# Kernel optimization log

Measured on AMD Instinct MI355X. Metric: run time of the kernel, lower is better.

## Reference

```python
import jax, jax.numpy as jnp
import numpy as np

N = 50000          # num nodes
DEG = 16           # fixed degree (uniform CSR)
E = N * DEG        # num edges
R = 8              # num relations
IN = 128
HID = 128
OUT = 40
BN_EPS = 1e-5


def setup_inputs() -> dict:
    key = jax.random.key(0)
    k = jax.random.split(key, 5)
    x = jax.random.normal(k[0], (N, IN), jnp.float32)
    # glorot-ish init for per-relation weights
    W1 = jax.random.normal(k[1], (R, IN, HID), jnp.float32) * (2.0 / (IN + HID)) ** 0.5
    W2 = jax.random.normal(k[2], (R, HID, OUT), jnp.float32) * (2.0 / (HID + OUT)) ** 0.5
    ptr = jnp.arange(N + 1, dtype=jnp.int32) * DEG            # CSR row offsets
    idx = jax.random.randint(k[3], (E,), 0, N, jnp.int32)     # neighbor (src) ids
    edge_types = jax.random.randint(k[4], (E,), 0, R, jnp.int32)
    return {
        "x": x, "W1": W1, "W2": W2,
        "bn_gamma": jnp.ones((HID,), jnp.float32),
        "bn_beta": jnp.zeros((HID,), jnp.float32),
        "bn_mean": jnp.zeros((HID,), jnp.float32),
        "bn_var": jnp.ones((HID,), jnp.float32),
        "ptr": ptr, "idx": idx, "edge_types": edge_types,
    }


def _rgcn_layer(h, W, ptr, idx, edge_types):
    # RGCNOP: out[i] = sum_{e in [ptr[i],ptr[i+1])} x[idx[e]] @ W[etype[e]]
    # Efficient form: transform every node by every relation once, then gather
    # the (src, etype) pair per edge and scatter-add into destinations.
    xr = jnp.einsum('nd,rdh->nrh', h, W)             # [N, R, H]
    msgs = xr[idx, edge_types]                       # [E, H] irregular gather
    deg = ptr[1:] - ptr[:-1]                         # [N]
    dst = jnp.repeat(jnp.arange(ptr.shape[0] - 1, dtype=jnp.int32), deg,
                     total_repeat_length=idx.shape[0])
    agg = jax.ops.segment_sum(msgs, dst, num_segments=ptr.shape[0] - 1)
    return agg / deg[:, None].astype(agg.dtype)      # degree normalization


def reference(x, W1, W2, bn_gamma, bn_beta, bn_mean, bn_var, ptr, idx, edge_types):
    h = _rgcn_layer(x, W1, ptr, idx, edge_types)
    # BatchNorm1d in eval mode (history_size=0, dropout inactive)
    h = (h - bn_mean) * jax.lax.rsqrt(bn_var + BN_EPS) * bn_gamma + bn_beta
    h = jax.nn.relu(h)
    h = _rgcn_layer(h, W2, ptr, idx, edge_types)
    return jax.nn.log_softmax(h, axis=-1)
```

## Files before the change

### kernel.cpp

```cpp
#include <hip/hip_runtime.h>
#include <math.h>

typedef __attribute__((ext_vector_type(8))) short bf16x8;
typedef __attribute__((ext_vector_type(4))) float f32x4;

constexpr int kN   = 50000;
constexpr int kR   = 8;
constexpr int kIn  = 128;
constexpr int kHid = 128;
constexpr int kOut = 40;
constexpr int kNT  = 16;
constexpr int kLds = 1032;
constexpr float kBnEps = 1e-5f;

__device__ inline ushort f2bf(float x) {
    uint u = __float_as_uint(x);
    u += 0x7FFFu + ((u >> 16) & 1u);
    return (ushort)(u >> 16);
}
__device__ inline float bf2f(ushort s) { return __uint_as_float(((uint)s) << 16); }
__device__ inline ushort f2bf_c(float x) {
    return (ushort)((__float_as_uint(x) + 0x8000u) >> 16);
}


__global__ __launch_bounds__(256)
void prep_new(const float* __restrict__ x,  ushort* __restrict__ xb,
              const float* __restrict__ W1, ushort* __restrict__ W1p,
              const float* __restrict__ W2, ushort* __restrict__ W2p)
{
    const int b   = blockIdx.x;
    const int tid = threadIdx.x;
    if (b < 3125) {
        const size_t i = ((size_t)b * 256 + tid) * 8;
        const float4 v0 = *(const float4*)&x[i];
        const float4 v1 = *(const float4*)&x[i + 4];
        *(ushort4*)&xb[i]     = make_ushort4(f2bf(v0.x), f2bf(v0.y), f2bf(v0.z), f2bf(v0.w));
        *(ushort4*)&xb[i + 4] = make_ushort4(f2bf(v1.x), f2bf(v1.y), f2bf(v1.z), f2bf(v1.w));
        return;
    }
    const int lane = tid & 63;
    const int m = lane & 15, q = lane >> 4;
    ushort hv[8];
    if (b < 3125 + 64) {
        const int f  = (b - 3125) * 4 + (tid >> 6);
        const int nt = f >> 2, kt = f & 3;
        const int n  = nt * 16 + m;
        const int r  = n >> 7, h = n & 127;
        #pragma unroll
        for (int j = 0; j < 8; ++j) {
            const int k = kt * 32 + q * 8 + j;
            hv[j] = f2bf(W1[(size_t)r * 16384 + (size_t)k * 128 + h]);
        }
        const size_t o = ((size_t)f * 64 + lane) * 8;
        *(ushort4*)&W1p[o]     = make_ushort4(hv[0], hv[1], hv[2], hv[3]);
        *(ushort4*)&W1p[o + 4] = make_ushort4(hv[4], hv[5], hv[6], hv[7]);
    } else {
        const int f  = (b - 3189) * 4 + (tid >> 6);
        const int nt = f >> 2, kt = f & 3;
        const int n  = nt * 16 + m;
        const int r  = n >> 6, h = n & 63;
        #pragma unroll
        for (int j = 0; j < 8; ++j) {
            const int k = kt * 32 + q * 8 + j;
            hv[j] = (h < kOut) ? f2bf(W2[(size_t)r * 5120 + (size_t)k * 40 + h])
                               : (ushort)0;
        }
        const size_t o = ((size_t)f * 64 + lane) * 8;
        *(ushort4*)&W2p[o]     = make_ushort4(hv[0], hv[1], hv[2], hv[3]);
        *(ushort4*)&W2p[o + 4] = make_ushort4(hv[4], hv[5], hv[6], hv[7]);
    }
}

#define LOADA(MT,KT) const bf16x8 af##MT##KT = \
    *(const bf16x8*)&As[MT * 16 + m][KT * 32 + q * 8];

template<int NTW, int NCOLS>
__global__ __launch_bounds__(512, 4)
void xform(const ushort* __restrict__ in,
           const ushort* __restrict__ Bp,
           ushort* __restrict__ outp)
{
    __shared__ ushort As[64][136];
    const int tid  = threadIdx.x;
    const int base = blockIdx.x * 64;

    {
        const int row = tid >> 3, c = tid & 7;
        const int gr  = base + row;
        bf16x8 v0 = {0,0,0,0,0,0,0,0}, v1 = {0,0,0,0,0,0,0,0};
        if (gr < kN) {
            v0 = *(const bf16x8*)&in[(size_t)gr * 128 + c * 8];
            v1 = *(const bf16x8*)&in[(size_t)gr * 128 + c * 8 + 64];
        }
        *(bf16x8*)&As[row][c * 8]      = v0;
        *(bf16x8*)&As[row][c * 8 + 64] = v1;
    }
    __syncthreads();

    const int lane = tid & 63, wid = tid >> 6;
    const int m = lane & 15, q = lane >> 4;

    LOADA(0,0) LOADA(0,1) LOADA(0,2) LOADA(0,3)
    LOADA(1,0) LOADA(1,1) LOADA(1,2) LOADA(1,3)
    LOADA(2,0) LOADA(2,1) LOADA(2,2) LOADA(2,3)
    LOADA(3,0) LOADA(3,1) LOADA(3,2) LOADA(3,3)

    const bf16x8* B8 = (const bf16x8*)Bp;

    #pragma unroll
    for (int ii = 0; ii < NTW; ++ii) {
        const int nt = wid * NTW + ii;
        const bf16x8 b0 = B8[(size_t)(nt * 4 + 0) * 64 + lane];
        const bf16x8 b1 = B8[(size_t)(nt * 4 + 1) * 64 + lane];
        const bf16x8 b2 = B8[(size_t)(nt * 4 + 2) * 64 + lane];
        const bf16x8 b3 = B8[(size_t)(nt * 4 + 3) * 64 + lane];
        f32x4 c0 = {0.f,0.f,0.f,0.f}, c1 = {0.f,0.f,0.f,0.f};
        f32x4 c2 = {0.f,0.f,0.f,0.f}, c3 = {0.f,0.f,0.f,0.f};
        c0 = __builtin_amdgcn_mfma_f32_16x16x32_bf16(af00, b0, c0, 0, 0, 0);
        c1 = __builtin_amdgcn_mfma_f32_16x16x32_bf16(af10, b0, c1, 0, 0, 0);
        c2 = __builtin_amdgcn_mfma_f32_16x16x32_bf16(af20, b0, c2, 0, 0, 0);
        c3 = __builtin_amdgcn_mfma_f32_16x16x32_bf16(af30, b0, c3, 0, 0, 0);
        c0 = __builtin_amdgcn_mfma_f32_16x16x32_bf16(af01, b1, c0, 0, 0, 0);
        c1 = __builtin_amdgcn_mfma_f32_16x16x32_bf16(af11, b1, c1, 0, 0, 0);
        c2 = __builtin_amdgcn_mfma_f32_16x16x32_bf16(af21, b1, c2, 0, 0, 0);
        c3 = __builtin_amdgcn_mfma_f32_16x16x32_bf16(af31, b1, c3, 0, 0, 0);
        c0 = __builtin_amdgcn_mfma_f32_16x16x32_bf16(af02, b2, c0, 0, 0, 0);
        c1 = __builtin_amdgcn_mfma_f32_16x16x32_bf16(af12, b2, c1, 0, 0, 0);
        c2 = __builtin_amdgcn_mfma_f32_16x16x32_bf16(af22, b2, c2, 0, 0, 0);
        c3 = __builtin_amdgcn_mfma_f32_16x16x32_bf16(af32, b2, c3, 0, 0, 0);
        c0 = __builtin_amdgcn_mfma_f32_16x16x32_bf16(af03, b3, c0, 0, 0, 0);
        c1 = __builtin_amdgcn_mfma_f32_16x16x32_bf16(af13, b3, c1, 0, 0, 0);
        c2 = __builtin_amdgcn_mfma_f32_16x16x32_bf16(af23, b3, c2, 0, 0, 0);
        c3 = __builtin_amdgcn_mfma_f32_16x16x32_bf16(af33, b3, c3, 0, 0, 0);

        const int col = nt * 16 + m;
        #define STORE_MT(CC, MT) {                                          \
            const int r0 = base + MT * 16 + q * 4;                          \
            _Pragma("unroll")                                               \
            for (int i2 = 0; i2 < 4; ++i2) {                                \
                const int rr = r0 + i2;                                     \
                if (rr < kN)                                                \
                    outp[(size_t)rr * NCOLS + col] = f2bf_c(CC[i2]);        \
            } }
        STORE_MT(c0, 0) STORE_MT(c1, 1) STORE_MT(c2, 2) STORE_MT(c3, 3)
        #undef STORE_MT
    }
}

#define GADD(BV, GJ) \
    const uint BV = xrU[(size_t)(GJ) * 64 + lane]; \
    ax += __uint_as_float((BV) << 16); \
    ay += __uint_as_float((BV) & 0xffff0000u);

__global__ __launch_bounds__(512, 4)
void agg_bn(const ushort* __restrict__ xr1,
            const int* __restrict__ ptr, const int* __restrict__ idx,
            const int* __restrict__ etype,
            const float* __restrict__ gamma, const float* __restrict__ beta,
            const float* __restrict__ mean,  const float* __restrict__ var,
            ushort* __restrict__ h1b)
{
    const int lane = threadIdx.x & 63;
    const int wid  = threadIdx.x >> 6;
    const int node = blockIdx.x * 8 + wid;
    const int p0 = ptr[node], p1 = ptr[node + 1];
    const int deg = p1 - p0;
    const uint* xrU = (const uint*)xr1;

    float ax = 0.f, ay = 0.f;
    if (deg == 16) {
        const int gv = (idx[p0 + (lane & 15)] << 3) | etype[p0 + (lane & 15)];
        const int g0  = __builtin_amdgcn_readlane(gv, 0);
        const int g1  = __builtin_amdgcn_readlane(gv, 1);
        const int g2  = __builtin_amdgcn_readlane(gv, 2);
        const int g3  = __builtin_amdgcn_readlane(gv, 3);
        const int g4  = __builtin_amdgcn_readlane(gv, 4);
        const int g5  = __builtin_amdgcn_readlane(gv, 5);
        const int g6  = __builtin_amdgcn_readlane(gv, 6);
        const int g7  = __builtin_amdgcn_readlane(gv, 7);
        const int g8  = __builtin_amdgcn_readlane(gv, 8);
        const int g9  = __builtin_amdgcn_readlane(gv, 9);
        const int g10 = __builtin_amdgcn_readlane(gv, 10);
        const int g11 = __builtin_amdgcn_readlane(gv, 11);
        const int g12 = __builtin_amdgcn_readlane(gv, 12);
        const int g13 = __builtin_amdgcn_readlane(gv, 13);
        const int g14 = __builtin_amdgcn_readlane(gv, 14);
        const int g15 = __builtin_amdgcn_readlane(gv, 15);
        GADD(b0,  g0)  GADD(b1,  g1)  GADD(b2,  g2)  GADD(b3,  g3)
        GADD(b4,  g4)  GADD(b5,  g5)  GADD(b6,  g6)  GADD(b7,  g7)
        GADD(b8,  g8)  GADD(b9,  g9)  GADD(b10, g10) GADD(b11, g11)
        GADD(b12, g12) GADD(b13, g13) GADD(b14, g14) GADD(b15, g15)
    } else {
        for (int e = p0; e < p1; ++e) {
            const int src = __builtin_amdgcn_readfirstlane(idx[e]);
            const int et  = __builtin_amdgcn_readfirstlane(etype[e]);
            const uint b  = xrU[((size_t)src * 8 + et) * 64 + lane];
            ax += __uint_as_float(b << 16);
            ay += __uint_as_float(b & 0xffff0000u);
        }
    }

    const float invd = 1.0f / (float)deg;
    const int c0 = lane * 2;
    const float2 gm = *(const float2*)&gamma[c0];
    const float2 bt = *(const float2*)&beta[c0];
    const float2 mu = *(const float2*)&mean[c0];
    const float2 vr = *(const float2*)&var[c0];
    float v0 = (ax * invd - mu.x) * (gm.x * rsqrtf(vr.x + kBnEps)) + bt.x;
    float v1 = (ay * invd - mu.y) * (gm.y * rsqrtf(vr.y + kBnEps)) + bt.y;
    v0 = fmaxf(v0, 0.f);
    v1 = fmaxf(v1, 0.f);
    const uint px = (__float_as_uint(v0) + 0x8000u) >> 16;
    const uint py = (__float_as_uint(v1) + 0x8000u) & 0xffff0000u;
    ((uint*)h1b)[(size_t)node * 64 + lane] = px | py;
}

#define GADD2(BV, GJ) \
    const uint BV = xrU[(size_t)(GJ) * 32 + lane]; \
    ax += __uint_as_float((BV) << 16); \
    ay += __uint_as_float((BV) & 0xffff0000u);

__global__ __launch_bounds__(512, 4)
void agg_sm(const ushort* __restrict__ xr2,
            const int* __restrict__ ptr, const int* __restrict__ idx,
            const int* __restrict__ etype,
            float* __restrict__ out)
{
    const int lane = threadIdx.x & 63;
    const int wid  = threadIdx.x >> 6;
    const int node = blockIdx.x * 8 + wid;
    const int p0 = ptr[node], p1 = ptr[node + 1];
    const int deg = p1 - p0;
    const uint* xrU = (const uint*)xr2;

    float ax = 0.f, ay = 0.f;
    if (deg == 16) {
        const int gv = (idx[p0 + (lane & 15)] << 3) | etype[p0 + (lane & 15)];
        const int g0  = __builtin_amdgcn_readlane(gv, 0);
        const int g1  = __builtin_amdgcn_readlane(gv, 1);
        const int g2  = __builtin_amdgcn_readlane(gv, 2);
        const int g3  = __builtin_amdgcn_readlane(gv, 3);
        const int g4  = __builtin_amdgcn_readlane(gv, 4);
        const int g5  = __builtin_amdgcn_readlane(gv, 5);
        const int g6  = __builtin_amdgcn_readlane(gv, 6);
        const int g7  = __builtin_amdgcn_readlane(gv, 7);
        const int g8  = __builtin_amdgcn_readlane(gv, 8);
        const int g9  = __builtin_amdgcn_readlane(gv, 9);
        const int g10 = __builtin_amdgcn_readlane(gv, 10);
        const int g11 = __builtin_amdgcn_readlane(gv, 11);
        const int g12 = __builtin_amdgcn_readlane(gv, 12);
        const int g13 = __builtin_amdgcn_readlane(gv, 13);
        const int g14 = __builtin_amdgcn_readlane(gv, 14);
        const int g15 = __builtin_amdgcn_readlane(gv, 15);
        if (lane < 20) {
            GADD2(b0,  g0)  GADD2(b1,  g1)  GADD2(b2,  g2)  GADD2(b3,  g3)
            GADD2(b4,  g4)  GADD2(b5,  g5)  GADD2(b6,  g6)  GADD2(b7,  g7)
            GADD2(b8,  g8)  GADD2(b9,  g9)  GADD2(b10, g10) GADD2(b11, g11)
            GADD2(b12, g12) GADD2(b13, g13) GADD2(b14, g14) GADD2(b15, g15)
        }
    } else {
        for (int e = p0; e < p1; ++e) {
            const int src = __builtin_amdgcn_readfirstlane(idx[e]);
            const int et  = __builtin_amdgcn_readfirstlane(etype[e]);
            if (lane < 20) {
                const uint b = xrU[((size_t)src * 8 + et) * 32 + lane];
                ax += __uint_as_float(b << 16);
                ay += __uint_as_float(b & 0xffff0000u);
            }
        }
    }

    const float invd = 1.0f / (float)deg;
    ax *= invd; ay *= invd;

    float mx = (lane < 20) ? fmaxf(ax, ay) : -INFINITY;
    #pragma unroll
    for (int off = 32; off > 0; off >>= 1)
        mx = fmaxf(mx, __shfl_xor(mx, off, 64));
    float s = (lane < 20) ? (__expf(ax - mx) + __expf(ay - mx)) : 0.f;
    #pragma unroll
    for (int off = 32; off > 0; off >>= 1)
        s += __shfl_xor(s, off, 64);
    const float ls = __logf(s);
    if (lane < 20) {
        float2 o;
        o.x = ax - mx - ls;
        o.y = ay - mx - ls;
        *(float2*)&out[(size_t)node * kOut + lane * 2] = o;
    }
}


__device__ __forceinline__ void pack_unit(const float* __restrict__ W,
                                          ushort* __restrict__ dst,
                                          int N, int frag, int lane)
{
    const int kt = frag & 31;
    const int nt = frag >> 5;
    const int n  = nt * 16 + (lane & 15);
    const int q  = lane >> 4;
    ushort hv[8];
    #pragma unroll
    for (int j = 0; j < 8; ++j) {
        const int k = kt * 32 + q * 8 + j;
        hv[j] = f2bf((n < N) ? W[(size_t)k * N + n] : 0.f);
    }
    const size_t o = ((size_t)frag * 64 + lane) * 8;
    *(ushort4*)&dst[o]     = make_ushort4(hv[0], hv[1], hv[2], hv[3]);
    *(ushort4*)&dst[o + 4] = make_ushort4(hv[4], hv[5], hv[6], hv[7]);
}

__global__ __launch_bounds__(256)
void prep_old(const float* __restrict__ x,  ushort* __restrict__ xb,
              const float* __restrict__ W1, ushort* __restrict__ W1hi,
              const float* __restrict__ W2, ushort* __restrict__ W2hi)
{
    const int b   = blockIdx.x;
    const int tid = threadIdx.x;
    if (b < 3125) {
        const size_t i = ((size_t)b * 256 + tid) * 8;
        const float4 v0 = *(const float4*)&x[i];
        const float4 v1 = *(const float4*)&x[i + 4];
        *(ushort4*)&xb[i]     = make_ushort4(f2bf(v0.x), f2bf(v0.y), f2bf(v0.z), f2bf(v0.w));
        *(ushort4*)&xb[i + 4] = make_ushort4(f2bf(v1.x), f2bf(v1.y), f2bf(v1.z), f2bf(v1.w));
    } else if (b < 3125 + 64) {
        pack_unit(W1, W1hi, kHid, (b - 3125) * 4 + (tid >> 6), tid & 63);
    } else {
        const int frag = (b - 3189) * 4 + (tid >> 6);
        if (frag < 96) pack_unit(W2, W2hi, kOut, frag, tid & 63);
    }
}

#define ACCUM_ET(ET, VX, VY)                                   \
    if      ((ET) == 0) { a0.x += (VX); a0.y += (VY); }        \
    else if ((ET) == 1) { a1.x += (VX); a1.y += (VY); }        \
    else if ((ET) == 2) { a2.x += (VX); a2.y += (VY); }        \
    else if ((ET) == 3) { a3.x += (VX); a3.y += (VY); }        \
    else if ((ET) == 4) { a4.x += (VX); a4.y += (VY); }        \
    else if ((ET) == 5) { a5.x += (VX); a5.y += (VY); }        \
    else if ((ET) == 6) { a6.x += (VX); a6.y += (VY); }        \
    else                { a7.x += (VX); a7.y += (VY); }

#define GATHER(BV, SRC) \
    const ushort2 BV = *(const ushort2*)&feat[(size_t)(SRC) * 128 + d2];

#define ACCUM_EDGE(J, BV) \
    { const int et = __builtin_amdgcn_readlane(ve, J); ACCUM_ET(et, bf2f(BV.x), bf2f(BV.y)) }

#define STORE_AGG(RR, AV) \
    *(ushort2*)&aggHi[n][(RR) * 128 + d2] = make_ushort2(f2bf(AV.x), f2bf(AV.y));

__device__ __forceinline__ void phaseA_bf16(const ushort* __restrict__ feat,
                                            const int* __restrict__ ptr,
                                            const int* __restrict__ idx,
                                            const int* __restrict__ etype,
                                            int base, ushort (*aggHi)[kLds])
{
    const int lane = threadIdx.x & 63;
    const int wid  = threadIdx.x >> 6;
    const int d2   = lane * 2;

    #pragma unroll
    for (int t = 0; t < 2; ++t) {
        const int n    = wid * 2 + t;
        const int node = base + n;
        const int p0   = ptr[node];
        const int deg  = ptr[node + 1] - p0;

        float2 a0 = {0.f,0.f}, a1 = {0.f,0.f}, a2 = {0.f,0.f}, a3 = {0.f,0.f};
        float2 a4 = {0.f,0.f}, a5 = {0.f,0.f}, a6 = {0.f,0.f}, a7 = {0.f,0.f};

        if (deg == 16) {
            const int vi = idx[p0 + (lane & 15)];
            const int ve = etype[p0 + (lane & 15)];
            const int s0  = __builtin_amdgcn_readlane(vi, 0);
            const int s1  = __builtin_amdgcn_readlane(vi, 1);
            const int s2  = __builtin_amdgcn_readlane(vi, 2);
            const int s3  = __builtin_amdgcn_readlane(vi, 3);
            const int s4  = __builtin_amdgcn_readlane(vi, 4);
            const int s5  = __builtin_amdgcn_readlane(vi, 5);
            const int s6  = __builtin_amdgcn_readlane(vi, 6);
            const int s7  = __builtin_amdgcn_readlane(vi, 7);
            const int s8  = __builtin_amdgcn_readlane(vi, 8);
            const int s9  = __builtin_amdgcn_readlane(vi, 9);
            const int s10 = __builtin_amdgcn_readlane(vi, 10);
            const int s11 = __builtin_amdgcn_readlane(vi, 11);
            const int s12 = __builtin_amdgcn_readlane(vi, 12);
            const int s13 = __builtin_amdgcn_readlane(vi, 13);
            const int s14 = __builtin_amdgcn_readlane(vi, 14);
            const int s15 = __builtin_amdgcn_readlane(vi, 15);
            GATHER(b0,  s0)  GATHER(b1,  s1)  GATHER(b2,  s2)  GATHER(b3,  s3)
            GATHER(b4,  s4)  GATHER(b5,  s5)  GATHER(b6,  s6)  GATHER(b7,  s7)
            GATHER(b8,  s8)  GATHER(b9,  s9)  GATHER(b10, s10) GATHER(b11, s11)
            GATHER(b12, s12) GATHER(b13, s13) GATHER(b14, s14) GATHER(b15, s15)
            ACCUM_EDGE(0,  b0)  ACCUM_EDGE(1,  b1)  ACCUM_EDGE(2,  b2)  ACCUM_EDGE(3,  b3)
            ACCUM_EDGE(4,  b4)  ACCUM_EDGE(5,  b5)  ACCUM_EDGE(6,  b6)  ACCUM_EDGE(7,  b7)
            ACCUM_EDGE(8,  b8)  ACCUM_EDGE(9,  b9)  ACCUM_EDGE(10, b10) ACCUM_EDGE(11, b11)
            ACCUM_EDGE(12, b12) ACCUM_EDGE(13, b13) ACCUM_EDGE(14, b14) ACCUM_EDGE(15, b15)
        } else {
            for (int e = p0; e < p0 + deg; ++e) {
                const int src = __builtin_amdgcn_readfirstlane(idx[e]);
                const int et  = __builtin_amdgcn_readfirstlane(etype[e]);
                const ushort2 u = *(const ushort2*)&feat[(size_t)src * 128 + d2];
                ACCUM_ET(et, bf2f(u.x), bf2f(u.y))
            }
        }
        STORE_AGG(0, a0) STORE_AGG(1, a1) STORE_AGG(2, a2) STORE_AGG(3, a3)
        STORE_AGG(4, a4) STORE_AGG(5, a5) STORE_AGG(6, a6) STORE_AGG(7, a7)
    }
}

__global__ __launch_bounds__(512, 4)
void rgcn_layer1(const ushort* __restrict__ xb,
                 const ushort* __restrict__ W1hi,
                 const float* __restrict__ gamma, const float* __restrict__ beta,
                 const float* __restrict__ mean,  const float* __restrict__ var,
                 const int* __restrict__ ptr, const int* __restrict__ idx,
                 const int* __restrict__ etype,
                 ushort* __restrict__ h1b)
{
    __shared__ ushort aggHi[kNT][kLds];
    const int tid  = threadIdx.x;
    const int base = blockIdx.x * kNT;

    phaseA_bf16(xb, ptr, idx, etype, base, aggHi);
    __syncthreads();

    const int lane = tid & 63;
    const int wid  = tid >> 6;
    const int m    = lane & 15;
    const int q    = lane >> 4;

    const bf16x8* Bh = (const bf16x8*)W1hi + (size_t)wid * 32 * 64 + lane;
    f32x4 acc = {0.f, 0.f, 0.f, 0.f};

    #pragma unroll 4
    for (int kt = 0; kt < 32; ++kt) {
        const bf16x8 ah = *(const bf16x8*)&aggHi[m][kt * 32 + q * 8];
        const bf16x8 bh = Bh[(size_t)kt * 64];
        acc = __builtin_amdgcn_mfma_f32_16x16x32_bf16(ah, bh, acc, 0, 0, 0);
    }

    const int c = wid * 16 + m;
    const float g  = gamma[c] * rsqrtf(var[c] + kBnEps);
    const float mu = mean[c];
    const float bt = beta[c];
    #pragma unroll
    for (int i = 0; i < 4; ++i) {
        const int node = base + q * 4 + i;
        const float invdeg = 1.0f / (float)(ptr[node + 1] - ptr[node]);
        float v = (acc[i] * invdeg - mu) * g + bt;
        v = fmaxf(v, 0.f);
        h1b[(size_t)node * kHid + c] = f2bf(v);
    }
}

__global__ __launch_bounds__(512, 4)
void rgcn_layer2(const ushort* __restrict__ h1b,
                 const ushort* __restrict__ W2hi,
                 const int* __restrict__ ptr, const int* __restrict__ idx,
                 const int* __restrict__ etype,
                 float* __restrict__ out)
{
    __shared__ ushort aggHi[kNT][kLds];
    __shared__ float logits[kNT][48];
    const int tid  = threadIdx.x;
    const int base = blockIdx.x * kNT;

    phaseA_bf16(h1b, ptr, idx, etype, base, aggHi);
    __syncthreads();

    const int lane = tid & 63;
    const int wid  = tid >> 6;
    const int m    = lane & 15;
    const int q    = lane >> 4;

    if (wid < 3) {
        const bf16x8* Bh = (const bf16x8*)W2hi + (size_t)wid * 32 * 64 + lane;
        f32x4 acc = {0.f, 0.f, 0.f, 0.f};
        #pragma unroll 4
        for (int kt = 0; kt < 32; ++kt) {
            const bf16x8 ah = *(const bf16x8*)&aggHi[m][kt * 32 + q * 8];
            const bf16x8 bh = Bh[(size_t)kt * 64];
            acc = __builtin_amdgcn_mfma_f32_16x16x32_bf16(ah, bh, acc, 0, 0, 0);
        }
        const int n = wid * 16 + m;
        if (n < kOut) {
            #pragma unroll
            for (int i = 0; i < 4; ++i) {
                const int node = base + q * 4 + i;
                const float invdeg = 1.0f / (float)(ptr[node + 1] - ptr[node]);
                logits[q * 4 + i][n] = acc[i] * invdeg;
            }
        }
    }
    __syncthreads();

    #pragma unroll
    for (int i = 0; i < 2; ++i) {
        const int nrow = wid * 2 + i;
        const int node = base + nrow;
        const float v = (lane < kOut) ? logits[nrow][lane] : -INFINITY;
        float mx = v;
        #pragma unroll
        for (int off = 32; off > 0; off >>= 1)
            mx = fmaxf(mx, __shfl_xor(mx, off, 64));
        float s = (lane < kOut) ? __expf(v - mx) : 0.f;
        #pragma unroll
        for (int off = 32; off > 0; off >>= 1)
            s += __shfl_xor(s, off, 64);
        if (lane < kOut)
            out[(size_t)node * kOut + lane] = v - mx - __logf(s);
    }
}

extern "C" void kernel_launch(void* const* d_in, const int* in_sizes, int n_in,
                              void* d_out, int out_size, void* d_ws, size_t ws_size,
                              hipStream_t stream)
{
    const float* x     = (const float*)d_in[0];
    const float* W1    = (const float*)d_in[1];
    const float* W2    = (const float*)d_in[2];
    const float* gamma = (const float*)d_in[3];
    const float* beta  = (const float*)d_in[4];
    const float* mean  = (const float*)d_in[5];
    const float* var   = (const float*)d_in[6];
    const int*   ptr   = (const int*)d_in[7];
    const int*   idx   = (const int*)d_in[8];
    const int*   et    = (const int*)d_in[9];
    float*       out   = (float*)d_out;

    char* ws = (char*)d_ws;
    constexpr size_t kNeedNew = 128393216;

    if (ws_size >= kNeedNew) {
        ushort* xb  = (ushort*)ws;
        ushort* h1b = (ushort*)(ws + 12800000);
        ushort* W1p = (ushort*)(ws + 25600000);
        ushort* W2p = (ushort*)(ws + 25862144);
        ushort* xr  = (ushort*)(ws + 25993216);

        prep_new<<<dim3(3125 + 64 + 32), dim3(256), 0, stream>>>(x, xb, W1, W1p, W2, W2p);
        xform<8, 1024><<<dim3(782), dim3(512), 0, stream>>>(xb, W1p, xr);
        agg_bn<<<dim3(6250), dim3(512), 0, stream>>>(xr, ptr, idx, et,
                                                     gamma, beta, mean, var, h1b);
        xform<4, 512><<<dim3(782), dim3(512), 0, stream>>>(h1b, W2p, xr);
        agg_sm<<<dim3(6250), dim3(512), 0, stream>>>(xr, ptr, idx, et, out);
    } else {
        ushort* h1b  = (ushort*)ws;
        ushort* xb   = (ushort*)(ws + 12800000);
        ushort* W1hi = (ushort*)(ws + 25600000);
        ushort* W2hi = (ushort*)(ws + 25600000 + 262144);

        prep_old<<<dim3(3125 + 64 + 24), dim3(256), 0, stream>>>(x, xb, W1, W1hi, W2, W2hi);
        dim3 grid(kN / kNT), block(512);
        rgcn_layer1<<<grid, block, 0, stream>>>(xb, W1hi, gamma, beta, mean, var,
                                                ptr, idx, et, h1b);
        rgcn_layer2<<<grid, block, 0, stream>>>(h1b, W2hi, ptr, idx, et, out);
    }
}
```

Baseline: 212.9 us.

## Stage xform outputs through LDS for coalesced stores; two nodes per wave in agg_bn

The transform kernel now writes MFMA results into a padded LDS tile and then stores each 128-column slab to global memory as 16-byte vectors per thread, replacing scattered 2-byte stores. Its column-tile loop is reordered so all eight waves cover one contiguous 128-column slab per iteration. The first aggregation kernel handles two nodes per wave, issuing 32 independent gathers before accumulating, which raises memory-level parallelism and halves the grid. The cost is two block barriers per slab in xform, extra LDS, and higher register pressure in agg_bn.

```diff
diff --git a/kernel.cpp b/kernel.cpp
--- a/kernel.cpp
+++ b/kernel.cpp
@@ -3,6 +3,7 @@
 
 typedef __attribute__((ext_vector_type(8))) short bf16x8;
 typedef __attribute__((ext_vector_type(4))) float f32x4;
+typedef __attribute__((ext_vector_type(2))) unsigned long long u64x2;
 
 constexpr int kN   = 50000;
 constexpr int kR   = 8;
@@ -75,13 +76,16 @@
 #define LOADA(MT,KT) const bf16x8 af##MT##KT = \
     *(const bf16x8*)&As[MT * 16 + m][KT * 32 + q * 8];
 
-template<int NTW, int NCOLS>
-__global__ __launch_bounds__(512, 4)
-void xform(const ushort* __restrict__ in,
-           const ushort* __restrict__ Bp,
-           ushort* __restrict__ outp)
-{
+template<int NCOLS>
+__device__ __forceinline__ void xform_body(const ushort* __restrict__ in,
+                                           const ushort* __restrict__ Bp,
+                                           ushort* __restrict__ outp)
+{
+    constexpr int G = NCOLS / 128;
     __shared__ ushort As[64][136];
+    __shared__ unsigned long long Cs64[64 * 33];
+    ushort* Cs = (ushort*)Cs64;
+
     const int tid  = threadIdx.x;
     const int base = blockIdx.x * 64;
 
@@ -107,10 +111,12 @@
     LOADA(3,0) LOADA(3,1) LOADA(3,2) LOADA(3,3)
 
     const bf16x8* B8 = (const bf16x8*)Bp;
-
-    #pragma unroll
-    for (int ii = 0; ii < NTW; ++ii) {
-        const int nt = wid * NTW + ii;
+    const int srow = tid >> 3, scc = (tid & 7) * 16;
+    const int sgr  = base + srow;
+
+    #pragma unroll 1
+    for (int ii = 0; ii < G; ++ii) {
+        const int nt = ii * 8 + wid;
         const bf16x8 b0 = B8[(size_t)(nt * 4 + 0) * 64 + lane];
         const bf16x8 b1 = B8[(size_t)(nt * 4 + 1) * 64 + lane];
         const bf16x8 b2 = B8[(size_t)(nt * 4 + 2) * 64 + lane];
@@ -134,24 +140,43 @@
         c2 = __builtin_amdgcn_mfma_f32_16x16x32_bf16(af23, b3, c2, 0, 0, 0);
         c3 = __builtin_amdgcn_mfma_f32_16x16x32_bf16(af33, b3, c3, 0, 0, 0);
 
-        const int col = nt * 16 + m;
-        #define STORE_MT(CC, MT) {                                          \
-            const int r0 = base + MT * 16 + q * 4;                          \
-            _Pragma("unroll")                                               \
-            for (int i2 = 0; i2 < 4; ++i2) {                                \
-                const int rr = r0 + i2;                                     \
-                if (rr < kN)                                                \
-                    outp[(size_t)rr * NCOLS + col] = f2bf_c(CC[i2]);        \
-            } }
-        STORE_MT(c0, 0) STORE_MT(c1, 1) STORE_MT(c2, 2) STORE_MT(c3, 3)
-        #undef STORE_MT
-    }
-}
-
-#define GADD(BV, GJ) \
-    const uint BV = xrU[(size_t)(GJ) * 64 + lane]; \
-    ax += __uint_as_float((BV) << 16); \
-    ay += __uint_as_float((BV) & 0xffff0000u);
+        #pragma unroll
+        for (int i2 = 0; i2 < 4; ++i2) {
+            Cs[(0 * 16 + q * 4 + i2) * 132 + wid * 16 + m] = f2bf_c(c0[i2]);
+            Cs[(1 * 16 + q * 4 + i2) * 132 + wid * 16 + m] = f2bf_c(c1[i2]);
+            Cs[(2 * 16 + q * 4 + i2) * 132 + wid * 16 + m] = f2bf_c(c2[i2]);
+            Cs[(3 * 16 + q * 4 + i2) * 132 + wid * 16 + m] = f2bf_c(c3[i2]);
+        }
+        __syncthreads();
+        const unsigned long long* s =
+            (const unsigned long long*)&Cs[srow * 132 + scc];
+        const unsigned long long v0_ = s[0], v1_ = s[1], v2_ = s[2], v3_ = s[3];
+        __syncthreads();
+        if (sgr < kN) {
+            unsigned long long* d =
+                (unsigned long long*)&outp[(size_t)sgr * NCOLS + ii * 128 + scc];
+            u64x2 p0; p0.x = v0_; p0.y = v1_;
+            u64x2 p1; p1.x = v2_; p1.y = v3_;
+            *(u64x2*)d       = p0;
+            *(u64x2*)(d + 2) = p1;
+        }
+    }
+}
+
+__global__ __launch_bounds__(512, 4)
+void xform_l1(const ushort* __restrict__ in, const ushort* __restrict__ Bp,
+              ushort* __restrict__ outp)
+{ xform_body<1024>(in, Bp, outp); }
+
+__global__ __launch_bounds__(512, 4)
+void xform_l2(const ushort* __restrict__ in, const ushort* __restrict__ Bp,
+              ushort* __restrict__ outp)
+{ xform_body<512>(in, Bp, outp); }
+
+#define RLG(J)  const int g##J = __builtin_amdgcn_readlane(gv, J);
+#define LDU(B, J) const uint B = xrU[(size_t)g##J * 64 + lane];
+#define ACC2(AX, AY, B) { AX += __uint_as_float((B) << 16); \
+                          AY += __uint_as_float((B) & 0xffff0000u); }
 
 __global__ __launch_bounds__(512, 4)
 void agg_bn(const ushort* __restrict__ xr1,
@@ -163,57 +188,74 @@
 {
     const int lane = threadIdx.x & 63;
     const int wid  = threadIdx.x >> 6;
-    const int node = blockIdx.x * 8 + wid;
-    const int p0 = ptr[node], p1 = ptr[node + 1];
-    const int deg = p1 - p0;
+    const int nA   = blockIdx.x * 16 + wid * 2;
+    const int p0 = ptr[nA], p1 = ptr[nA + 1], p2 = ptr[nA + 2];
+    const int degA = p1 - p0, degB = p2 - p1;
     const uint* xrU = (const uint*)xr1;
 
-    float ax = 0.f, ay = 0.f;
-    if (deg == 16) {
-        const int gv = (idx[p0 + (lane & 15)] << 3) | etype[p0 + (lane & 15)];
-        const int g0  = __builtin_amdgcn_readlane(gv, 0);
-        const int g1  = __builtin_amdgcn_readlane(gv, 1);
-        const int g2  = __builtin_amdgcn_readlane(gv, 2);
-        const int g3  = __builtin_amdgcn_readlane(gv, 3);
-        const int g4  = __builtin_amdgcn_readlane(gv, 4);
-        const int g5  = __builtin_amdgcn_readlane(gv, 5);
-        const int g6  = __builtin_amdgcn_readlane(gv, 6);
-        const int g7  = __builtin_amdgcn_readlane(gv, 7);
-        const int g8  = __builtin_amdgcn_readlane(gv, 8);
-        const int g9  = __builtin_amdgcn_readlane(gv, 9);
-        const int g10 = __builtin_amdgcn_readlane(gv, 10);
-        const int g11 = __builtin_amdgcn_readlane(gv, 11);
-        const int g12 = __builtin_amdgcn_readlane(gv, 12);
-        const int g13 = __builtin_amdgcn_readlane(gv, 13);
-        const int g14 = __builtin_amdgcn_readlane(gv, 14);
-        const int g15 = __builtin_amdgcn_readlane(gv, 15);
-        GADD(b0,  g0)  GADD(b1,  g1)  GADD(b2,  g2)  GADD(b3,  g3)
-        GADD(b4,  g4)  GADD(b5,  g5)  GADD(b6,  g6)  GADD(b7,  g7)
-        GADD(b8,  g8)  GADD(b9,  g9)  GADD(b10, g10) GADD(b11, g11)
-        GADD(b12, g12) GADD(b13, g13) GADD(b14, g14) GADD(b15, g15)
+    float axA = 0.f, ayA = 0.f, axB = 0.f, ayB = 0.f;
+    if (degA == 16 && degB == 16) {
+        const int gv = (idx[p0 + (lane & 31)] << 3) | etype[p0 + (lane & 31)];
+        RLG(0)  RLG(1)  RLG(2)  RLG(3)  RLG(4)  RLG(5)  RLG(6)  RLG(7)
+        RLG(8)  RLG(9)  RLG(10) RLG(11) RLG(12) RLG(13) RLG(14) RLG(15)
+        RLG(16) RLG(17) RLG(18) RLG(19) RLG(20) RLG(21) RLG(22) RLG(23)
+        RLG(24) RLG(25) RLG(26) RLG(27) RLG(28) RLG(29) RLG(30) RLG(31)
+        LDU(bA0,  0)  LDU(bA1,  1)  LDU(bA2,  2)  LDU(bA3,  3)
+        LDU(bA4,  4)  LDU(bA5,  5)  LDU(bA6,  6)  LDU(bA7,  7)
+        LDU(bA8,  8)  LDU(bA9,  9)  LDU(bA10, 10) LDU(bA11, 11)
+        LDU(bA12, 12) LDU(bA13, 13) LDU(bA14, 14) LDU(bA15, 15)
+        LDU(bB0,  16) LDU(bB1,  17) LDU(bB2,  18) LDU(bB3,  19)
+        LDU(bB4,  20) LDU(bB5,  21) LDU(bB6,  22) LDU(bB7,  23)
+        LDU(bB8,  24) LDU(bB9,  25) LDU(bB10, 26) LDU(bB11, 27)
+        LDU(bB12, 28) LDU(bB13, 29) LDU(bB14, 30) LDU(bB15, 31)
+        ACC2(axA, ayA, bA0)  ACC2(axA, ayA, bA1)  ACC2(axA, ayA, bA2)
+        ACC2(axA, ayA, bA3)  ACC2(axA, ayA, bA4)  ACC2(axA, ayA, bA5)
+        ACC2(axA, ayA, bA6)  ACC2(axA, ayA, bA7)  ACC2(axA, ayA, bA8)
+        ACC2(axA, ayA, bA9)  ACC2(axA, ayA, bA10) ACC2(axA, ayA, bA11)
+        ACC2(axA, ayA, bA12) ACC2(axA, ayA, bA13) ACC2(axA, ayA, bA14)
+        ACC2(axA, ayA, bA15)
+        ACC2(axB, ayB, bB0)  ACC2(axB, ayB, bB1)  ACC2(axB, ayB, bB2)
+        ACC2(axB, ayB, bB3)  ACC2(axB, ayB, bB4)  ACC2(axB, ayB, bB5)
+        ACC2(axB, ayB, bB6)  ACC2(axB, ayB, bB7)  ACC2(axB, ayB, bB8)
+        ACC2(axB, ayB, bB9)  ACC2(axB, ayB, bB10) ACC2(axB, ayB, bB11)
+        ACC2(axB, ayB, bB12) ACC2(axB, ayB, bB13) ACC2(axB, ayB, bB14)
+        ACC2(axB, ayB, bB15)
     } else {
         for (int e = p0; e < p1; ++e) {
             const int src = __builtin_amdgcn_readfirstlane(idx[e]);
             const int et  = __builtin_amdgcn_readfirstlane(etype[e]);
             const uint b  = xrU[((size_t)src * 8 + et) * 64 + lane];
-            ax += __uint_as_float(b << 16);
-            ay += __uint_as_float(b & 0xffff0000u);
-        }
-    }
-
-    const float invd = 1.0f / (float)deg;
+            ACC2(axA, ayA, b)
+        }
+        for (int e = p1; e < p2; ++e) {
+            const int src = __builtin_amdgcn_readfirstlane(idx[e]);
+            const int et  = __builtin_amdgcn_readfirstlane(etype[e]);
+            const uint b  = xrU[((size_t)src * 8 + et) * 64 + lane];
+            ACC2(axB, ayB, b)
+        }
+    }
+
     const int c0 = lane * 2;
     const float2 gm = *(const float2*)&gamma[c0];
     const float2 bt = *(const float2*)&beta[c0];
     const float2 mu = *(const float2*)&mean[c0];
     const float2 vr = *(const float2*)&var[c0];
-    float v0 = (ax * invd - mu.x) * (gm.x * rsqrtf(vr.x + kBnEps)) + bt.x;
-    float v1 = (ay * invd - mu.y) * (gm.y * rsqrtf(vr.y + kBnEps)) + bt.y;
-    v0 = fmaxf(v0, 0.f);
-    v1 = fmaxf(v1, 0.f);
-    const uint px = (__float_as_uint(v0) + 0x8000u) >> 16;
-    const uint py = (__float_as_uint(v1) + 0x8000u) & 0xffff0000u;
-    ((uint*)h1b)[(size_t)node * 64 + lane] = px | py;
+    const float gx = gm.x * rsqrtf(vr.x + kBnEps);
+    const float gy = gm.y * rsqrtf(vr.y + kBnEps);
+    const float iA = 1.0f / (float)degA;
+    const float iB = 1.0f / (float)degB;
+
+    float v0 = fmaxf((axA * iA - mu.x) * gx + bt.x, 0.f);
+    float v1 = fmaxf((ayA * iA - mu.y) * gy + bt.y, 0.f);
+    uint px = (__float_as_uint(v0) + 0x8000u) >> 16;
+    uint py = (__float_as_uint(v1) + 0x8000u) & 0xffff0000u;
+    ((uint*)h1b)[(size_t)nA * 64 + lane] = px | py;
+
+    v0 = fmaxf((axB * iB - mu.x) * gx + bt.x, 0.f);
+    v1 = fmaxf((ayB * iB - mu.y) * gy + bt.y, 0.f);
+    px = (__float_as_uint(v0) + 0x8000u) >> 16;
+    py = (__float_as_uint(v1) + 0x8000u) & 0xffff0000u;
+    ((uint*)h1b)[(size_t)(nA + 1) * 64 + lane] = px | py;
 }
 
 #define GADD2(BV, GJ) \
@@ -542,10 +584,10 @@
         ushort* xr  = (ushort*)(ws + 25993216);
 
         prep_new<<<dim3(3125 + 64 + 32), dim3(256), 0, stream>>>(x, xb, W1, W1p, W2, W2p);
-        xform<8, 1024><<<dim3(782), dim3(512), 0, stream>>>(xb, W1p, xr);
-        agg_bn<<<dim3(6250), dim3(512), 0, stream>>>(xr, ptr, idx, et,
+        xform_l1<<<dim3(782), dim3(512), 0, stream>>>(xb, W1p, xr);
+        agg_bn<<<dim3(3125), dim3(512), 0, stream>>>(xr, ptr, idx, et,
                                                      gamma, beta, mean, var, h1b);
-        xform<4, 512><<<dim3(782), dim3(512), 0, stream>>>(h1b, W2p, xr);
+        xform_l2<<<dim3(782), dim3(512), 0, stream>>>(h1b, W2p, xr);
         agg_sm<<<dim3(6250), dim3(512), 0, stream>>>(xr, ptr, idx, et, out);
     } else {
         ushort* h1b  = (ushort*)ws;
```

Measured after the change: 200.3 us. 5.9% less time.
